# Kernel tuning notes

Hardware: AMD Instinct MI355X
Metric: run time of the kernel (lower is better)

## Reference

```python
import jax, jax.numpy as jnp
import numpy as np

B, N, E = 16, 10000, 160000
C_IN, C_SP, C_OUT = 32, 16, 32


def _glorot(key, shape):
    s = float(np.sqrt(6.0 / (shape[0] + shape[1])))
    return jax.random.uniform(key, shape, jnp.float32, -s, s)


def setup_inputs() -> dict:
    key = jax.random.key(0)
    ks = jax.random.split(key, 12)
    X = jax.random.normal(ks[0], (B, N, C_IN), jnp.float32)
    edge_index1 = jax.random.randint(ks[1], (2, E), 0, N)
    edge_weight1 = jax.random.uniform(ks[2], (E,), jnp.float32)
    res_n_id1 = jnp.arange(N)
    edge_index2 = jax.random.randint(ks[3], (2, E), 0, N)
    edge_weight2 = jax.random.uniform(ks[4], (E,), jnp.float32)
    res_n_id2 = jnp.arange(N)
    # conv1 params (in=C_IN, out=C_SP, edge_channels=1, concat=True)
    amp_w1 = _glorot(ks[5], (1, C_IN))            # [edge_ch, in]
    gate_w1 = _glorot(ks[6], (2 * C_IN + 1, 1))   # Linear(2*in+edge_ch, 1)
    gate_b1 = jnp.zeros((1,), jnp.float32)
    w1 = _glorot(ks[7], (2 * C_IN, C_SP))         # concat weight
    b1 = jnp.zeros((C_SP,), jnp.float32)
    # conv2 params (in=C_SP, out=C_OUT)
    amp_w2 = _glorot(ks[8], (1, C_SP))
    gate_w2 = _glorot(ks[9], (2 * C_SP + 1, 1))
    gate_b2 = jnp.zeros((1,), jnp.float32)
    w2 = _glorot(ks[10], (2 * C_SP, C_OUT))
    b2 = jnp.zeros((C_OUT,), jnp.float32)
    return dict(X=X, edge_index1=edge_index1, edge_weight1=edge_weight1, res_n_id1=res_n_id1,
                edge_index2=edge_index2, edge_weight2=edge_weight2, res_n_id2=res_n_id2,
                amp_w1=amp_w1, gate_w1=gate_w1, gate_b1=gate_b1, w1=w1, b1=b1,
                amp_w2=amp_w2, gate_w2=gate_w2, gate_b2=gate_b2, w2=w2, b2=b2)


def _sagela(x_src, x_dst, edge_index, edge_weight, amp_w, gate_w, gate_b, w, b):
    # x_src: [B, N_src, C], x_dst: [B, N_dst, C]
    src, dst = edge_index[0], edge_index[1]
    n_dst = x_dst.shape[1]
    C = x_src.shape[-1]
    x_j = x_src[:, src]                       # [B, E, C] gathered source feats
    x_i = x_dst[:, dst]                       # [B, E, C] gathered target feats
    e = edge_weight[:, None]                  # [E, 1] edge features
    # gate_linear(cat[x_i, x_j, e]) split into three matmuls (same math)
    wg_i, wg_j, wg_e = gate_w[:C], gate_w[C:2 * C], gate_w[2 * C:]
    lamb = jax.nn.sigmoid(x_i @ wg_i + x_j @ wg_j + (e @ wg_e)[None] + gate_b)  # [B, E, 1]
    amp = e @ amp_w                           # [E, C] edge amplification
    msg = amp[None, :, :] * x_j * lamb        # [B, E, C]
    # mean aggregation over incoming edges (scatter-add / count)
    aggr = jnp.zeros((x_src.shape[0], n_dst, C), msg.dtype).at[:, dst].add(msg)
    cnt = jnp.zeros((n_dst,), msg.dtype).at[dst].add(1.0)
    aggr = aggr / jnp.maximum(cnt, 1.0)[None, :, None]
    out = jnp.concatenate([x_dst, aggr], axis=-1) @ w + b  # [B, N_dst, out]
    return out


def reference(X, edge_index1, edge_weight1, res_n_id1, edge_index2, edge_weight2, res_n_id2,
              amp_w1, gate_w1, gate_b1, w1, b1, amp_w2, gate_w2, gate_b2, w2, b2):
    h = _sagela(X, X[:, res_n_id1], edge_index1, edge_weight1, amp_w1, gate_w1, gate_b1, w1, b1)
    h = jax.nn.leaky_relu(h, 0.01)
    out = _sagela(h, h[:, res_n_id2], edge_index2, edge_weight2, amp_w2, gate_w2, gate_b2, w2, b2)
    return out
```

## Files before the change

kernel.cpp:

```cpp
#include <hip/hip_runtime.h>
#include <math.h>

#define B 16
#define N 10000
#define E 160000
#define CAP 96

__device__ __forceinline__ ushort f2bf(float v) {
    uint u = __float_as_uint(v);
    u = (u + 0x7fffu + ((u >> 16) & 1u)) >> 16;
    return (ushort)u;
}
__device__ __forceinline__ float bf2f(ushort u) { return __uint_as_float(((uint)u) << 16); }
__device__ __forceinline__ float bf2f_lo(uint u) { return __uint_as_float(u << 16); }
__device__ __forceinline__ float bf2f_hi(uint u) { return __uint_as_float(u & 0xffff0000u); }
__device__ __forceinline__ float dec_ew(uint u) {
    return ((float)(u >> 14) + 0.5f) * (1.0f / 262144.0f);
}

__global__ __launch_bounds__(256)
void prep_bucket_kernel(const float* __restrict__ X,
                        const float* __restrict__ gate_w1,
                        const float* __restrict__ amp_w1,
                        const float* __restrict__ b1,
                        const int* __restrict__ ei1, const float* __restrict__ ew1,
                        const int* __restrict__ ei2, const float* __restrict__ ew2,
                        const float* __restrict__ w1,
                        const float* __restrict__ w2,
                        ushort* __restrict__ yt,
                        float* __restrict__ xpart,
                        float* __restrict__ gi, float* __restrict__ gj,
                        float* __restrict__ w2T,
                        int* __restrict__ bcount1, uint* __restrict__ bucket1,
                        int* __restrict__ bcount2, uint* __restrict__ bucket2) {
    __shared__ __align__(16) float s_w1[64 * 16];
    int tid = threadIdx.x;
    {
        int i = tid * 4;
        *(float4*)&s_w1[i] = *(const float4*)&w1[i];
    }
    __syncthreads();

    int gtid = blockIdx.x * 256 + tid;
    int gs = gridDim.x * 256;

    for (int t = gtid; t < 2 * E; t += gs) {
        if (t < E) {
            int d = ei1[E + t];
            int pos = atomicAdd(&bcount1[d], 1);
            if (pos < CAP) {
                uint q = (uint)(ew1[t] * 262144.0f);
                if (q > 262143u) q = 262143u;
                bucket1[d * CAP + pos] = (q << 14) | (uint)ei1[t];
            }
        } else {
            int e = t - E;
            int d = ei2[E + e];
            int pos = atomicAdd(&bcount2[d], 1);
            if (pos < CAP) {
                uint q = (uint)(ew2[e] * 262144.0f);
                if (q > 262143u) q = 262143u;
                bucket2[d * CAP + pos] = (q << 14) | (uint)ei2[e];
            }
        }
    }

    if (gtid < 1024) {
        w2T[(gtid & 31) * 32 + (gtid >> 5)] = w2[gtid];
    }

    for (int tile = blockIdx.x; tile < N / 16; tile += gridDim.x) {
        int n0 = tile * 16;
        int nl = tid >> 4, b = tid & 15;
        int n = n0 + nl;
        const float4* xr4 = (const float4*)(X + ((size_t)b * N + n) * 32);
        float4 xr[8];
        #pragma unroll
        for (int q = 0; q < 8; ++q) xr[q] = xr4[q];
        const float* xs = (const float*)xr;

        float pi = 0.f, pj = 0.f;
        #pragma unroll
        for (int q = 0; q < 8; ++q) {
            float4 v = xr[q];
            pi += v.x * gate_w1[4*q]   + v.y * gate_w1[4*q+1]
                + v.z * gate_w1[4*q+2] + v.w * gate_w1[4*q+3];
            pj += v.x * gate_w1[32+4*q]   + v.y * gate_w1[32+4*q+1]
                + v.z * gate_w1[32+4*q+2] + v.w * gate_w1[32+4*q+3];
        }

        float po[16], py[16];
        #pragma unroll
        for (int o = 0; o < 16; ++o) { po[o] = b1[o]; py[o] = 0.f; }
        #pragma unroll
        for (int c = 0; c < 32; ++c) {
            float xa = xs[c];
            float ya = amp_w1[c] * xa;
            const float4* wa = (const float4*)&s_w1[c * 16];
            const float4* wb = (const float4*)&s_w1[(32 + c) * 16];
            #pragma unroll
            for (int q = 0; q < 4; ++q) {
                float4 a = wa[q], bb = wb[q];
                po[4*q]   += xa * a.x;  py[4*q]   += ya * bb.x;
                po[4*q+1] += xa * a.y;  py[4*q+1] += ya * bb.y;
                po[4*q+2] += xa * a.z;  py[4*q+2] += ya * bb.z;
                po[4*q+3] += xa * a.w;  py[4*q+3] += ya * bb.w;
            }
        }

        int r = n0 * 16 + tid;
        uint pk[8];
        #pragma unroll
        for (int j = 0; j < 8; ++j)
            pk[j] = (uint)f2bf(py[2*j]) | ((uint)f2bf(py[2*j+1]) << 16);
        uint4* yd = (uint4*)(yt + (size_t)r * 16);
        yd[0] = make_uint4(pk[0], pk[1], pk[2], pk[3]);
        yd[1] = make_uint4(pk[4], pk[5], pk[6], pk[7]);
        float4* xd = (float4*)(xpart + (size_t)r * 16);
        #pragma unroll
        for (int q = 0; q < 4; ++q)
            xd[q] = make_float4(po[4*q], po[4*q+1], po[4*q+2], po[4*q+3]);
        gi[r] = pi; gj[r] = pj;
    }
}

__global__ __launch_bounds__(256, 8)
void agg1_kernel(const uint4* __restrict__ y4,
                 const float* __restrict__ xpart,
                 const float* __restrict__ gi,
                 const float* __restrict__ gj,
                 const int* __restrict__ bcount,
                 const uint* __restrict__ bucket,
                 const float* __restrict__ gate_w,
                 const float* __restrict__ gate_b,
                 const float* __restrict__ gate_w2,
                 ushort* __restrict__ htb,
                 float* __restrict__ gi2, float* __restrict__ gj2) {
    __shared__ uint  s_eb[CAP];
    __shared__ float s_coef[CAP * 16];
    __shared__ float s_gi[16];

    int n = blockIdx.x;
    int tid = threadIdx.x;

    int cnt = bcount[n];
    int deg = cnt < CAP ? cnt : CAP;
    if (tid < CAP / 4)
        ((uint4*)s_eb)[tid] = ((const uint4*)(bucket + (size_t)n * CAP))[tid];
    if (tid < 16) s_gi[tid] = gi[n * 16 + tid] + gate_b[0];
    __syncthreads();

    float wge = gate_w[64];
    for (int p = tid; p < deg * 16; p += 256) {
        int k = p >> 4, b = p & 15;
        uint pr = s_eb[k];
        float w = dec_ew(pr);
        float z = s_gi[b] + gj[(pr & 0x3FFFu) * 16 + b] + w * wge;
        s_coef[p] = w / (1.0f + __expf(-z));
    }
    __syncthreads();

    int wv = tid >> 6, l = tid & 63;
    int og = l & 1;
    int b  = 4 * wv + ((l >> 1) & 3);
    int h  = l >> 3;
    uint boff = (uint)b * 2 + og;
    float a0 = 0.f, a1 = 0.f, a2 = 0.f, a3 = 0.f;
    float a4 = 0.f, a5 = 0.f, a6 = 0.f, a7 = 0.f;
    for (int k = h; k < deg; k += 8) {
        uint pr = s_eb[k];
        float cc = s_coef[(k << 4) | b];
        uint4 u = y4[(pr & 0x3FFFu) * 32u + boff];
        a0 += cc * bf2f_lo(u.x); a1 += cc * bf2f_hi(u.x);
        a2 += cc * bf2f_lo(u.y); a3 += cc * bf2f_hi(u.y);
        a4 += cc * bf2f_lo(u.z); a5 += cc * bf2f_hi(u.z);
        a6 += cc * bf2f_lo(u.w); a7 += cc * bf2f_hi(u.w);
    }
    a0 += __shfl_xor(a0, 8, 64); a0 += __shfl_xor(a0, 16, 64); a0 += __shfl_xor(a0, 32, 64);
    a1 += __shfl_xor(a1, 8, 64); a1 += __shfl_xor(a1, 16, 64); a1 += __shfl_xor(a1, 32, 64);
    a2 += __shfl_xor(a2, 8, 64); a2 += __shfl_xor(a2, 16, 64); a2 += __shfl_xor(a2, 32, 64);
    a3 += __shfl_xor(a3, 8, 64); a3 += __shfl_xor(a3, 16, 64); a3 += __shfl_xor(a3, 32, 64);
    a4 += __shfl_xor(a4, 8, 64); a4 += __shfl_xor(a4, 16, 64); a4 += __shfl_xor(a4, 32, 64);
    a5 += __shfl_xor(a5, 8, 64); a5 += __shfl_xor(a5, 16, 64); a5 += __shfl_xor(a5, 32, 64);
    a6 += __shfl_xor(a6, 8, 64); a6 += __shfl_xor(a6, 16, 64); a6 += __shfl_xor(a6, 32, 64);
    a7 += __shfl_xor(a7, 8, 64); a7 += __shfl_xor(a7, 16, 64); a7 += __shfl_xor(a7, 32, 64);

    if (h == 0) {
        float inv = 1.0f / fmaxf((float)cnt, 1.0f);
        size_t xb = ((size_t)n * 16 + b) * 16 + 8 * og;
        float4 xp0 = *(const float4*)&xpart[xb];
        float4 xp1 = *(const float4*)&xpart[xb + 4];
        float v0 = xp0.x + inv * a0, v1 = xp0.y + inv * a1;
        float v2 = xp0.z + inv * a2, v3 = xp0.w + inv * a3;
        float v4 = xp1.x + inv * a4, v5 = xp1.y + inv * a5;
        float v6 = xp1.z + inv * a6, v7 = xp1.w + inv * a7;
        v0 = v0 > 0.f ? v0 : 0.01f * v0;  v1 = v1 > 0.f ? v1 : 0.01f * v1;
        v2 = v2 > 0.f ? v2 : 0.01f * v2;  v3 = v3 > 0.f ? v3 : 0.01f * v3;
        v4 = v4 > 0.f ? v4 : 0.01f * v4;  v5 = v5 > 0.f ? v5 : 0.01f * v5;
        v6 = v6 > 0.f ? v6 : 0.01f * v6;  v7 = v7 > 0.f ? v7 : 0.01f * v7;
        uint4 pk;
        pk.x = (uint)f2bf(v0) | ((uint)f2bf(v1) << 16);
        pk.y = (uint)f2bf(v2) | ((uint)f2bf(v3) << 16);
        pk.z = (uint)f2bf(v4) | ((uint)f2bf(v5) << 16);
        pk.w = (uint)f2bf(v6) | ((uint)f2bf(v7) << 16);
        ((uint4*)htb)[(size_t)n * 32 + boff] = pk;
        int ob = 8 * og;
        float pi = v0 * gate_w2[ob]     + v1 * gate_w2[ob + 1]
                 + v2 * gate_w2[ob + 2] + v3 * gate_w2[ob + 3]
                 + v4 * gate_w2[ob + 4] + v5 * gate_w2[ob + 5]
                 + v6 * gate_w2[ob + 6] + v7 * gate_w2[ob + 7];
        float pj = v0 * gate_w2[16 + ob]     + v1 * gate_w2[16 + ob + 1]
                 + v2 * gate_w2[16 + ob + 2] + v3 * gate_w2[16 + ob + 3]
                 + v4 * gate_w2[16 + ob + 4] + v5 * gate_w2[16 + ob + 5]
                 + v6 * gate_w2[16 + ob + 6] + v7 * gate_w2[16 + ob + 7];
        pi += __shfl_xor(pi, 1, 64);
        pj += __shfl_xor(pj, 1, 64);
        if (og == 0) { gi2[n * 16 + b] = pi; gj2[n * 16 + b] = pj; }
    }
}

__global__ __launch_bounds__(256, 8)
void agg_dense2_kernel(const uint4* __restrict__ htb4,
                       const float* __restrict__ gi,
                       const float* __restrict__ gj,
                       const int* __restrict__ bcount,
                       const uint* __restrict__ bucket,
                       const float* __restrict__ gate_w,
                       const float* __restrict__ gate_b,
                       const float* __restrict__ amp_w,
                       const float* __restrict__ w2T,
                       const float* __restrict__ b2,
                       float* __restrict__ out) {
    __shared__ uint  s_eb[CAP];
    __shared__ float s_coef[CAP * 16];
    __shared__ float s_gi[16];
    __shared__ __align__(16) float s_x[16][20];
    __shared__ __align__(16) float s_feat[16][20];
    __shared__ __align__(16) float s_wmT[32 * 36];

    int n = blockIdx.x;
    int tid = threadIdx.x;

    int cnt = bcount[n];
    int deg = cnt < CAP ? cnt : CAP;
    if (tid < CAP / 4)
        ((uint4*)s_eb)[tid] = ((const uint4*)(bucket + (size_t)n * CAP))[tid];
    {
        int o = tid >> 3, k4 = tid & 7;
        *(float4*)&s_wmT[o * 36 + k4 * 4] = ((const float4*)w2T)[o * 8 + k4];
    }
    if (tid < 32) {
        uint4 u = htb4[(size_t)n * 32 + tid];
        int b = tid >> 1, cb = (tid & 1) * 8;
        float4 f0, f1;
        f0.x = bf2f_lo(u.x); f0.y = bf2f_hi(u.x);
        f0.z = bf2f_lo(u.y); f0.w = bf2f_hi(u.y);
        f1.x = bf2f_lo(u.z); f1.y = bf2f_hi(u.z);
        f1.z = bf2f_lo(u.w); f1.w = bf2f_hi(u.w);
        *(float4*)&s_x[b][cb]     = f0;
        *(float4*)&s_x[b][cb + 4] = f1;
    }
    if (tid < 16) s_gi[tid] = gi[n * 16 + tid] + gate_b[0];
    __syncthreads();

    float wge = gate_w[32];
    for (int p = tid; p < deg * 16; p += 256) {
        int k = p >> 4, b = p & 15;
        uint pr = s_eb[k];
        float w = dec_ew(pr);
        float z = s_gi[b] + gj[(pr & 0x3FFFu) * 16 + b] + w * wge;
        s_coef[p] = w / (1.0f + __expf(-z));
    }
    __syncthreads();

    int wv = tid >> 6, l = tid & 63;
    int c8 = l & 1;
    int b  = 4 * wv + ((l >> 1) & 3);
    int qd = l >> 3;
    uint boff = (uint)b * 2 + c8;
    float a0 = 0.f, a1 = 0.f, a2 = 0.f, a3 = 0.f;
    float a4 = 0.f, a5 = 0.f, a6 = 0.f, a7 = 0.f;
    int k = qd;
    for (; k + 8 < deg; k += 32) {
        bool v2 = (k + 16) < deg, v3 = (k + 24) < deg;
        uint i2 = v2 ? (uint)(k + 16) : 0u;
        uint i3 = v3 ? (uint)(k + 24) : 0u;
        uint p0 = s_eb[k], p1 = s_eb[k + 8], p2 = s_eb[i2], p3 = s_eb[i3];
        float c0 = s_coef[(k << 4) | b];
        float c1 = s_coef[((k + 8) << 4) | b];
        float c2 = s_coef[(i2 << 4) | b]; if (!v2) c2 = 0.f;
        float c3 = s_coef[(i3 << 4) | b]; if (!v3) c3 = 0.f;
        uint4 u0 = htb4[(p0 & 0x3FFFu) * 32u + boff];
        uint4 u1 = htb4[(p1 & 0x3FFFu) * 32u + boff];
        uint4 u2 = htb4[(p2 & 0x3FFFu) * 32u + boff];
        uint4 u3 = htb4[(p3 & 0x3FFFu) * 32u + boff];
        a0 += c0 * bf2f_lo(u0.x) + c1 * bf2f_lo(u1.x) + c2 * bf2f_lo(u2.x) + c3 * bf2f_lo(u3.x);
        a1 += c0 * bf2f_hi(u0.x) + c1 * bf2f_hi(u1.x) + c2 * bf2f_hi(u2.x) + c3 * bf2f_hi(u3.x);
        a2 += c0 * bf2f_lo(u0.y) + c1 * bf2f_lo(u1.y) + c2 * bf2f_lo(u2.y) + c3 * bf2f_lo(u3.y);
        a3 += c0 * bf2f_hi(u0.y) + c1 * bf2f_hi(u1.y) + c2 * bf2f_hi(u2.y) + c3 * bf2f_hi(u3.y);
        a4 += c0 * bf2f_lo(u0.z) + c1 * bf2f_lo(u1.z) + c2 * bf2f_lo(u2.z) + c3 * bf2f_lo(u3.z);
        a5 += c0 * bf2f_hi(u0.z) + c1 * bf2f_hi(u1.z) + c2 * bf2f_hi(u2.z) + c3 * bf2f_hi(u3.z);
        a6 += c0 * bf2f_lo(u0.w) + c1 * bf2f_lo(u1.w) + c2 * bf2f_lo(u2.w) + c3 * bf2f_lo(u3.w);
        a7 += c0 * bf2f_hi(u0.w) + c1 * bf2f_hi(u1.w) + c2 * bf2f_hi(u2.w) + c3 * bf2f_hi(u3.w);
    }
    if (k < deg) {
        uint pr = s_eb[k];
        float cc = s_coef[(k << 4) | b];
        uint4 u = htb4[(pr & 0x3FFFu) * 32u + boff];
        a0 += cc * bf2f_lo(u.x); a1 += cc * bf2f_hi(u.x);
        a2 += cc * bf2f_lo(u.y); a3 += cc * bf2f_hi(u.y);
        a4 += cc * bf2f_lo(u.z); a5 += cc * bf2f_hi(u.z);
        a6 += cc * bf2f_lo(u.w); a7 += cc * bf2f_hi(u.w);
    }
    a0 += __shfl_xor(a0, 8, 64); a0 += __shfl_xor(a0, 16, 64); a0 += __shfl_xor(a0, 32, 64);
    a1 += __shfl_xor(a1, 8, 64); a1 += __shfl_xor(a1, 16, 64); a1 += __shfl_xor(a1, 32, 64);
    a2 += __shfl_xor(a2, 8, 64); a2 += __shfl_xor(a2, 16, 64); a2 += __shfl_xor(a2, 32, 64);
    a3 += __shfl_xor(a3, 8, 64); a3 += __shfl_xor(a3, 16, 64); a3 += __shfl_xor(a3, 32, 64);
    a4 += __shfl_xor(a4, 8, 64); a4 += __shfl_xor(a4, 16, 64); a4 += __shfl_xor(a4, 32, 64);
    a5 += __shfl_xor(a5, 8, 64); a5 += __shfl_xor(a5, 16, 64); a5 += __shfl_xor(a5, 32, 64);
    a6 += __shfl_xor(a6, 8, 64); a6 += __shfl_xor(a6, 16, 64); a6 += __shfl_xor(a6, 32, 64);
    a7 += __shfl_xor(a7, 8, 64); a7 += __shfl_xor(a7, 16, 64); a7 += __shfl_xor(a7, 32, 64);
    if (qd == 0) {
        float inv = 1.0f / fmaxf((float)cnt, 1.0f);
        int cb = 8 * c8;
        s_feat[b][cb]     = a0 * amp_w[cb]     * inv;
        s_feat[b][cb + 1] = a1 * amp_w[cb + 1] * inv;
        s_feat[b][cb + 2] = a2 * amp_w[cb + 2] * inv;
        s_feat[b][cb + 3] = a3 * amp_w[cb + 3] * inv;
        s_feat[b][cb + 4] = a4 * amp_w[cb + 4] * inv;
        s_feat[b][cb + 5] = a5 * amp_w[cb + 5] * inv;
        s_feat[b][cb + 6] = a6 * amp_w[cb + 6] * inv;
        s_feat[b][cb + 7] = a7 * amp_w[cb + 7] * inv;
    }
    __syncthreads();

    {
        int o2 = tid & 15, bb = tid >> 4;
        const float4* wr0 = (const float4*)&s_wmT[(2 * o2) * 36];
        const float4* wr1 = (const float4*)&s_wmT[(2 * o2 + 1) * 36];
        const float4* x4  = (const float4*)&s_x[bb][0];
        const float4* f4  = (const float4*)&s_feat[bb][0];
        float d0 = b2[2 * o2], d1 = b2[2 * o2 + 1];
        #pragma unroll
        for (int q = 0; q < 4; ++q) {
            float4 xv = x4[q], fv = f4[q];
            float4 w0a = wr0[q], w0b = wr0[4 + q];
            float4 w1a = wr1[q], w1b = wr1[4 + q];
            d0 += xv.x * w0a.x + xv.y * w0a.y + xv.z * w0a.z + xv.w * w0a.w;
            d0 += fv.x * w0b.x + fv.y * w0b.y + fv.z * w0b.z + fv.w * w0b.w;
            d1 += xv.x * w1a.x + xv.y * w1a.y + xv.z * w1a.z + xv.w * w1a.w;
            d1 += fv.x * w1b.x + fv.y * w1b.y + fv.z * w1b.z + fv.w * w1b.w;
        }
        size_t ob = ((size_t)bb * N + n) * 32;
        float2 r; r.x = d0; r.y = d1;
        *(float2*)(out + ob + 2 * o2) = r;
    }
}

extern "C" void kernel_launch(void* const* d_in, const int* in_sizes, int n_in,
                              void* d_out, int out_size, void* d_ws, size_t ws_size,
                              hipStream_t stream) {
    const float* X       = (const float*)d_in[0];
    const int*   ei1     = (const int*)  d_in[1];
    const float* ew1     = (const float*)d_in[2];
    const int*   ei2     = (const int*)  d_in[4];
    const float* ew2     = (const float*)d_in[5];
    const float* amp_w1  = (const float*)d_in[7];
    const float* gate_w1 = (const float*)d_in[8];
    const float* gate_b1 = (const float*)d_in[9];
    const float* w1      = (const float*)d_in[10];
    const float* b1      = (const float*)d_in[11];
    const float* amp_w2  = (const float*)d_in[12];
    const float* gate_w2 = (const float*)d_in[13];
    const float* gate_b2 = (const float*)d_in[14];
    const float* w2      = (const float*)d_in[15];
    const float* b2      = (const float*)d_in[16];
    float* out = (float*)d_out;

    char* p = (char*)d_ws;
    ushort* yt     = (ushort*)p; p += (size_t)N * B * 16 * sizeof(ushort);
    ushort* htb    = (ushort*)p; p += (size_t)N * B * 16 * sizeof(ushort);
    float* xpart   = (float*)p;  p += (size_t)N * B * 16 * sizeof(float);
    float* gi1     = (float*)p;  p += (size_t)N * B * sizeof(float);
    float* gj1     = (float*)p;  p += (size_t)N * B * sizeof(float);
    float* gi2     = (float*)p;  p += (size_t)N * B * sizeof(float);
    float* gj2     = (float*)p;  p += (size_t)N * B * sizeof(float);
    uint*  bucket1 = (uint*)p;   p += (size_t)N * CAP * sizeof(uint);
    uint*  bucket2 = (uint*)p;   p += (size_t)N * CAP * sizeof(uint);
    int*   bcount1 = (int*)p;    p += (size_t)N * sizeof(int);
    int*   bcount2 = (int*)p;    p += (size_t)N * sizeof(int);
    float* w2T     = (float*)p;  p += 1024 * sizeof(float);

    hipMemsetAsync(bcount1, 0, 2 * (size_t)N * sizeof(int), stream);
    prep_bucket_kernel<<<2048, 256, 0, stream>>>(
        X, gate_w1, amp_w1, b1, ei1, ew1, ei2, ew2, w1, w2,
        yt, xpart, gi1, gj1, w2T,
        bcount1, bucket1, bcount2, bucket2);

    agg1_kernel<<<N, 256, 0, stream>>>(
        (const uint4*)yt, xpart, gi1, gj1, bcount1, bucket1,
        gate_w1, gate_b1, gate_w2, htb, gi2, gj2);

    agg_dense2_kernel<<<N, 256, 0, stream>>>(
        (const uint4*)htb, gi2, gj2, bcount2, bucket2,
        gate_w2, gate_b2, amp_w2, w2T, b2, out);
}
```

Measured before the change: 206.4 us.

## Split bucketing and row-prep into separate kernels with per-output-channel threads

Measured after the change: 201.9 us. -2.2%, faster.

```diff
diff --git a/kernel.cpp b/kernel.cpp
--- a/kernel.cpp
+++ b/kernel.cpp
@@ -19,29 +19,13 @@
 }
 
 __global__ __launch_bounds__(256)
-void prep_bucket_kernel(const float* __restrict__ X,
-                        const float* __restrict__ gate_w1,
-                        const float* __restrict__ amp_w1,
-                        const float* __restrict__ b1,
-                        const int* __restrict__ ei1, const float* __restrict__ ew1,
-                        const int* __restrict__ ei2, const float* __restrict__ ew2,
-                        const float* __restrict__ w1,
-                        const float* __restrict__ w2,
-                        ushort* __restrict__ yt,
-                        float* __restrict__ xpart,
-                        float* __restrict__ gi, float* __restrict__ gj,
-                        float* __restrict__ w2T,
-                        int* __restrict__ bcount1, uint* __restrict__ bucket1,
-                        int* __restrict__ bcount2, uint* __restrict__ bucket2) {
-    __shared__ __align__(16) float s_w1[64 * 16];
-    int tid = threadIdx.x;
-    {
-        int i = tid * 4;
-        *(float4*)&s_w1[i] = *(const float4*)&w1[i];
-    }
-    __syncthreads();
-
-    int gtid = blockIdx.x * 256 + tid;
+void bucket_kernel(const int* __restrict__ ei1, const float* __restrict__ ew1,
+                   const int* __restrict__ ei2, const float* __restrict__ ew2,
+                   const float* __restrict__ w2,
+                   float* __restrict__ w2T,
+                   int* __restrict__ bcount1, uint* __restrict__ bucket1,
+                   int* __restrict__ bcount2, uint* __restrict__ bucket2) {
+    int gtid = blockIdx.x * 256 + threadIdx.x;
     int gs = gridDim.x * 256;
 
     for (int t = gtid; t < 2 * E; t += gs) {
@@ -68,59 +52,61 @@
     if (gtid < 1024) {
         w2T[(gtid & 31) * 32 + (gtid >> 5)] = w2[gtid];
     }
-
-    for (int tile = blockIdx.x; tile < N / 16; tile += gridDim.x) {
-        int n0 = tile * 16;
-        int nl = tid >> 4, b = tid & 15;
-        int n = n0 + nl;
-        const float4* xr4 = (const float4*)(X + ((size_t)b * N + n) * 32);
-        float4 xr[8];
-        #pragma unroll
-        for (int q = 0; q < 8; ++q) xr[q] = xr4[q];
-        const float* xs = (const float*)xr;
-
-        float pi = 0.f, pj = 0.f;
-        #pragma unroll
-        for (int q = 0; q < 8; ++q) {
-            float4 v = xr[q];
-            pi += v.x * gate_w1[4*q]   + v.y * gate_w1[4*q+1]
-                + v.z * gate_w1[4*q+2] + v.w * gate_w1[4*q+3];
-            pj += v.x * gate_w1[32+4*q]   + v.y * gate_w1[32+4*q+1]
-                + v.z * gate_w1[32+4*q+2] + v.w * gate_w1[32+4*q+3];
-        }
-
-        float po[16], py[16];
-        #pragma unroll
-        for (int o = 0; o < 16; ++o) { po[o] = b1[o]; py[o] = 0.f; }
-        #pragma unroll
-        for (int c = 0; c < 32; ++c) {
-            float xa = xs[c];
-            float ya = amp_w1[c] * xa;
-            const float4* wa = (const float4*)&s_w1[c * 16];
-            const float4* wb = (const float4*)&s_w1[(32 + c) * 16];
-            #pragma unroll
-            for (int q = 0; q < 4; ++q) {
-                float4 a = wa[q], bb = wb[q];
-                po[4*q]   += xa * a.x;  py[4*q]   += ya * bb.x;
-                po[4*q+1] += xa * a.y;  py[4*q+1] += ya * bb.y;
-                po[4*q+2] += xa * a.z;  py[4*q+2] += ya * bb.z;
-                po[4*q+3] += xa * a.w;  py[4*q+3] += ya * bb.w;
-            }
-        }
-
-        int r = n0 * 16 + tid;
-        uint pk[8];
-        #pragma unroll
-        for (int j = 0; j < 8; ++j)
-            pk[j] = (uint)f2bf(py[2*j]) | ((uint)f2bf(py[2*j+1]) << 16);
-        uint4* yd = (uint4*)(yt + (size_t)r * 16);
-        yd[0] = make_uint4(pk[0], pk[1], pk[2], pk[3]);
-        yd[1] = make_uint4(pk[4], pk[5], pk[6], pk[7]);
-        float4* xd = (float4*)(xpart + (size_t)r * 16);
-        #pragma unroll
-        for (int q = 0; q < 4; ++q)
-            xd[q] = make_float4(po[4*q], po[4*q+1], po[4*q+2], po[4*q+3]);
-        gi[r] = pi; gj[r] = pj;
+}
+
+__global__ __launch_bounds__(256, 8)
+void rowprep_kernel(const float* __restrict__ X,
+                    const float* __restrict__ gate_w1,
+                    const float* __restrict__ amp_w1,
+                    const float* __restrict__ b1,
+                    const float* __restrict__ w1,
+                    ushort* __restrict__ yt,
+                    float* __restrict__ xpart,
+                    float* __restrict__ gi, float* __restrict__ gj) {
+    __shared__ __align__(16) float s_w1[64 * 16];
+    __shared__ float s_x[16][33];
+    __shared__ float s_py[16][17];
+
+    int n = blockIdx.x;
+    int tid = threadIdx.x;
+
+    {
+        int i = tid * 4;
+        *(float4*)&s_w1[i] = *(const float4*)&w1[i];
+    }
+    {
+        int b = tid >> 4, c2 = (tid & 15) * 2;
+        float2 v = *(const float2*)(X + ((size_t)b * N + n) * 32 + c2);
+        s_x[b][c2] = v.x; s_x[b][c2 + 1] = v.y;
+    }
+    __syncthreads();
+
+    int b = tid >> 4, o = tid & 15;
+    float po = b1[o], py = 0.f;
+    #pragma unroll
+    for (int c = 0; c < 32; ++c) {
+        float xa = s_x[b][c];
+        po += xa * s_w1[c * 16 + o];
+        py += amp_w1[c] * xa * s_w1[(32 + c) * 16 + o];
+    }
+    float pi = s_x[b][o] * gate_w1[o]      + s_x[b][o + 16] * gate_w1[o + 16];
+    float pj = s_x[b][o] * gate_w1[32 + o] + s_x[b][o + 16] * gate_w1[48 + o];
+    #pragma unroll
+    for (int off = 8; off; off >>= 1) {
+        pi += __shfl_xor(pi, off, 16);
+        pj += __shfl_xor(pj, off, 16);
+    }
+    int r = n * 16 + b;
+    xpart[(size_t)r * 16 + o] = po;
+    s_py[b][o] = py;
+    if (o == 0) { gi[r] = pi; gj[r] = pj; }
+    __syncthreads();
+
+    if (tid < 64) {
+        int bb = tid >> 2, j = tid & 3;
+        uint lo = (uint)f2bf(s_py[bb][4 * j])     | ((uint)f2bf(s_py[bb][4 * j + 1]) << 16);
+        uint hi = (uint)f2bf(s_py[bb][4 * j + 2]) | ((uint)f2bf(s_py[bb][4 * j + 3]) << 16);
+        ((uint2*)yt)[(size_t)(n * 16 + bb) * 4 + j] = make_uint2(lo, hi);
     }
 }
 
@@ -392,10 +378,12 @@
     float* w2T     = (float*)p;  p += 1024 * sizeof(float);
 
     hipMemsetAsync(bcount1, 0, 2 * (size_t)N * sizeof(int), stream);
-    prep_bucket_kernel<<<2048, 256, 0, stream>>>(
-        X, gate_w1, amp_w1, b1, ei1, ew1, ei2, ew2, w1, w2,
-        yt, xpart, gi1, gj1, w2T,
+    bucket_kernel<<<2048, 256, 0, stream>>>(
+        ei1, ew1, ei2, ew2, w2, w2T,
         bcount1, bucket1, bcount2, bucket2);
+
+    rowprep_kernel<<<N, 256, 0, stream>>>(
+        X, gate_w1, amp_w1, b1, w1, yt, xpart, gi1, gj1);
 
     agg1_kernel<<<N, 256, 0, stream>>>(
         (const uint4*)yt, xpart, gi1, gj1, bcount1, bucket1,
```
